# Optimization experiments

Measured on AMD Instinct MI355X. Metric: run time of the kernel, lower is better.

## Reference

```python
import jax, jax.numpy as jnp
import numpy as np

B, NX, NH, NY, K = 4096, 512, 512, 256, 8


def setup_inputs() -> dict:
    key = jax.random.key(0)
    k0, k1, k2, k3, k4, k5 = jax.random.split(key, 6)
    s = 1.0 / np.sqrt(NH)  # torch RNNCell init scale
    x = jax.random.normal(k0, (B, NX), jnp.float32)
    h = jax.random.normal(k1, (B, NH), jnp.float32)
    pi = jax.random.uniform(k2, (B, K), jnp.float32)
    pi = pi / pi.sum(axis=1, keepdims=True)  # __init_belief normalizes to sum 1
    W_ih = jax.random.uniform(k3, (K, NH, NX), jnp.float32, minval=-s, maxval=s)
    W_hh = jax.random.uniform(k4, (K, NH, NH), jnp.float32, minval=-s, maxval=s)
    W_out = jax.random.uniform(k5, (NY, NH), jnp.float32, minval=-s, maxval=s)
    return {"x": x, "h": h, "pi": pi, "W_ih": W_ih, "W_hh": W_hh, "W_out": W_out}


def reference(x, h, pi, W_ih, W_hh, W_out):
    # Per-state RNN cells (bias=False): h_k[:, :, k] = tanh(x @ W_ih[k].T + h @ W_hh[k].T)
    h_k = jnp.tanh(
        jnp.einsum('bx,knx->bnk', x, W_ih)
        + jnp.einsum('bh,knh->bnk', h, W_hh)
    )  # (B, NH, K)
    # out_k = out_layer applied per state: (B, NY, K)
    out_k = jnp.einsum('bnk,yn->byk', h_k, W_out)
    # belief-weighted soft combination of hidden states: states[b] = h_k[b] @ pi[b]
    h_mix = jnp.einsum('bnk,bk->bn', h_k, pi)  # (B, NH)
    out = h_mix @ W_out.T  # (B, NY)
    return (out, h_mix, out_k, h_k)
```

## Files before the change

### kernel.cpp

```cpp
#include <hip/hip_runtime.h>
#include <hip/hip_bf16.h>
#include <stdint.h>

typedef unsigned short u16;
typedef __attribute__((ext_vector_type(8))) short short8;
typedef __attribute__((ext_vector_type(4))) float f32x4;

#define BATCH 4096
#define OFF_OUT  0
#define OFF_HMIX (BATCH * 256)
#define OFF_OK   (OFF_HMIX + BATCH * 512)
#define OFF_HK   (OFF_OK + BATCH * 256 * 8)

#define WS_XB   0
#define WS_HB   (2097152)
#define WS_WIH  (4194304)
#define WS_WHH  (6291456)
#define WS_WOUT (8388608)
#define WS_T    (8519680)
#define WS_OB   (25296896)

__device__ __forceinline__ float b2f(u16 v) {
  union { uint32_t u; float f; } c; c.u = ((uint32_t)v) << 16; return c.f;
}
__device__ __forceinline__ u16 f2b(float f) {
  union { float f; uint32_t u; } c; c.f = f;
  uint32_t u = c.u;
  return (u16)((u + 0x7fffu + ((u >> 16) & 1u)) >> 16);
}

__device__ __forceinline__ void gload16(const u16* g, u16* l) {
  __builtin_amdgcn_global_load_lds(
      (const __attribute__((address_space(1))) void*)g,
      (__attribute__((address_space(3))) void*)l, 16, 0, 0);
}

__global__ __launch_bounds__(256) void k0_cvt(
    const float* __restrict__ x, const float* __restrict__ h,
    const float* __restrict__ Wih, const float* __restrict__ Whh,
    const float* __restrict__ Wout, u16* __restrict__ ws) {
  const int i = blockIdx.x * 256 + threadIdx.x;
  const float* src; int j; size_t dst;
  if      (i <  524288) { src = x;    j = i;           dst = WS_XB;   }
  else if (i < 1048576) { src = h;    j = i -  524288; dst = WS_HB;   }
  else if (i < 1572864) { src = Wih;  j = i - 1048576; dst = WS_WIH;  }
  else if (i < 2097152) { src = Whh;  j = i - 1572864; dst = WS_WHH;  }
  else                  { src = Wout; j = i - 2097152; dst = WS_WOUT; }
  const float4 v = ((const float4*)src)[j];
  ushort4 o;
  o.x = f2b(v.x); o.y = f2b(v.y); o.z = f2b(v.z); o.w = f2b(v.w);
  ((ushort4*)(ws + dst))[j] = o;
}

__global__ __launch_bounds__(256) void k1_gemm_tanh(
    const u16* __restrict__ xb, const u16* __restrict__ hb,
    const u16* __restrict__ Wih, const u16* __restrict__ Whh,
    u16* __restrict__ Tb) {
  __shared__ u16 S[128 * 136];
  u16* As = S;
  u16* Bs = S + 128 * 64;
  const int tid  = threadIdx.x;
  const int lane = tid & 63;
  const int w    = tid >> 6;
  const int wm   = w >> 1, wn = w & 1;
  const int row0 = blockIdx.x * 128;
  const int col0 = blockIdx.y * 128;
  const int kk   = col0 >> 9;
  const int nh0  = col0 & 511;
  const int sr   = tid >> 3;
  const int sc   = ((tid & 7) ^ ((tid >> 3) & 7)) * 8;
  const int ldsw = (w * 8) * 64;

  const u16* WihK = Wih + (size_t)kk * 512 * 512;
  const u16* WhhK = Whh + (size_t)kk * 512 * 512;

  f32x4 acc[4][4] = {};

  for (int kt = 0; kt < 16; ++kt) {
    const int kb = kt * 64;
    const u16* Asrc; const u16* Bsrc; int ko;
    if (kb < 512) { Asrc = xb; Bsrc = WihK; ko = kb; }
    else          { Asrc = hb; Bsrc = WhhK; ko = kb - 512; }
#pragma unroll
    for (int ro = 0; ro < 4; ++ro) {
      gload16(Asrc + (size_t)(row0 + ro * 32 + sr) * 512 + ko + sc, &As[ro * 32 * 64 + ldsw]);
      gload16(Bsrc + (size_t)(nh0  + ro * 32 + sr) * 512 + ko + sc, &Bs[ro * 32 * 64 + ldsw]);
    }
    __syncthreads();
    const int l7 = lane & 7, quad = lane >> 4, rl = lane & 15;
#pragma unroll
    for (int ks = 0; ks < 2; ++ks) {
      short8 af[4], bf[4];
      const int cs = ((ks * 4 + quad) ^ l7) * 8;
#pragma unroll
      for (int i = 0; i < 4; ++i)
        af[i] = *(const short8*)&As[(wm * 64 + i * 16 + rl) * 64 + cs];
#pragma unroll
      for (int j = 0; j < 4; ++j)
        bf[j] = *(const short8*)&Bs[(wn * 64 + j * 16 + rl) * 64 + cs];
#pragma unroll
      for (int i = 0; i < 4; ++i)
#pragma unroll
        for (int j = 0; j < 4; ++j)
          acc[i][j] = __builtin_amdgcn_mfma_f32_16x16x32_bf16(af[i], bf[j], acc[i][j], 0, 0, 0);
    }
    __syncthreads();
  }

  const int quad = lane >> 4, cl = lane & 15;
#pragma unroll
  for (int i = 0; i < 4; ++i)
#pragma unroll
    for (int j = 0; j < 4; ++j)
#pragma unroll
      for (int r = 0; r < 4; ++r) {
        const int row = wm * 64 + i * 16 + quad * 4 + r;
        const int col = wn * 64 + j * 16 + cl;
        const float v = acc[i][j][r];
        const float e = __expf(2.0f * v);
        S[row * 136 + col] = f2b(1.0f - 2.0f / (e + 1.0f));
      }
  __syncthreads();
#pragma unroll
  for (int it = 0; it < 8; ++it) {
    const int idx = it * 256 + tid;
    const int c = idx & 15;
    const int r = idx >> 4;
    *(short8*)&Tb[(size_t)(row0 + r) * 4096 + col0 + c * 8] =
        *(const short8*)&S[r * 136 + c * 8];
  }
}

__global__ __launch_bounds__(256) void k2_gemm_out(
    const u16* __restrict__ Tb, const u16* __restrict__ Wout,
    u16* __restrict__ Ob) {
  __shared__ u16 S[128 * 136];
  u16* As = S;
  u16* Bs = S + 128 * 64;
  const int tid  = threadIdx.x;
  const int lane = tid & 63;
  const int w    = tid >> 6;
  const int wm   = w >> 1, wn = w & 1;
  const int row0 = blockIdx.x * 128;
  const int y0   = blockIdx.y * 128;
  const int kk   = blockIdx.z;
  const int sr   = tid >> 3;
  const int sc   = ((tid & 7) ^ ((tid >> 3) & 7)) * 8;
  const int ldsw = (w * 8) * 64;

  f32x4 acc[4][4] = {};

  for (int kt = 0; kt < 8; ++kt) {
    const int kb = kt * 64;
#pragma unroll
    for (int ro = 0; ro < 4; ++ro) {
      gload16(Tb + (size_t)(row0 + ro * 32 + sr) * 4096 + kk * 512 + kb + sc,
              &As[ro * 32 * 64 + ldsw]);
      gload16(Wout + (size_t)(y0 + ro * 32 + sr) * 512 + kb + sc,
              &Bs[ro * 32 * 64 + ldsw]);
    }
    __syncthreads();
    const int l7 = lane & 7, quad = lane >> 4, rl = lane & 15;
#pragma unroll
    for (int ks = 0; ks < 2; ++ks) {
      short8 af[4], bf[4];
      const int cs = ((ks * 4 + quad) ^ l7) * 8;
#pragma unroll
      for (int i = 0; i < 4; ++i)
        af[i] = *(const short8*)&As[(wm * 64 + i * 16 + rl) * 64 + cs];
#pragma unroll
      for (int j = 0; j < 4; ++j)
        bf[j] = *(const short8*)&Bs[(wn * 64 + j * 16 + rl) * 64 + cs];
#pragma unroll
      for (int i = 0; i < 4; ++i)
#pragma unroll
        for (int j = 0; j < 4; ++j)
          acc[i][j] = __builtin_amdgcn_mfma_f32_16x16x32_bf16(af[i], bf[j], acc[i][j], 0, 0, 0);
    }
    __syncthreads();
  }

  const int quad = lane >> 4, cl = lane & 15;
#pragma unroll
  for (int i = 0; i < 4; ++i)
#pragma unroll
    for (int j = 0; j < 4; ++j)
#pragma unroll
      for (int r = 0; r < 4; ++r) {
        const int row = wm * 64 + i * 16 + quad * 4 + r;
        const int col = wn * 64 + j * 16 + cl;
        S[row * 136 + col] = f2b(acc[i][j][r]);
      }
  __syncthreads();
#pragma unroll
  for (int it = 0; it < 8; ++it) {
    const int idx = it * 256 + tid;
    const int c = idx & 15;
    const int r = idx >> 4;
    *(short8*)&Ob[(size_t)(row0 + r) * 2048 + kk * 256 + y0 + c * 8] =
        *(const short8*)&S[r * 136 + c * 8];
  }
}

__global__ __launch_bounds__(512) void k3_epi(const float* __restrict__ pi,
                                              const u16* __restrict__ Tb,
                                              const u16* __restrict__ Ob,
                                              float* __restrict__ dout) {
  const int b   = blockIdx.x;
  const int tid = threadIdx.x;

  float pif[8];
#pragma unroll
  for (int k = 0; k < 8; ++k) pif[k] = pi[b * 8 + k];

  float tv[8]; float hm = 0.0f;
#pragma unroll
  for (int k = 0; k < 8; ++k) {
    const float v = b2f(Tb[(size_t)b * 4096 + k * 512 + tid]);
    tv[k] = v; hm += pif[k] * v;
  }
  float4* tw = (float4*)&dout[OFF_HK + (size_t)b * 4096 + tid * 8];
  tw[0] = make_float4(tv[0], tv[1], tv[2], tv[3]);
  tw[1] = make_float4(tv[4], tv[5], tv[6], tv[7]);
  dout[OFF_HMIX + (size_t)b * 512 + tid] = hm;

  if (tid < 256) {
    float ov[8]; float om = 0.0f;
#pragma unroll
    for (int k = 0; k < 8; ++k) {
      const float v = b2f(Ob[(size_t)b * 2048 + k * 256 + tid]);
      ov[k] = v; om += pif[k] * v;
    }
    float4* ow = (float4*)&dout[OFF_OK + (size_t)b * 2048 + tid * 8];
    ow[0] = make_float4(ov[0], ov[1], ov[2], ov[3]);
    ow[1] = make_float4(ov[4], ov[5], ov[6], ov[7]);
    dout[OFF_OUT + (size_t)b * 256 + tid] = om;
  }
}

extern "C" void kernel_launch(void* const* d_in, const int* in_sizes, int n_in,
                              void* d_out, int out_size, void* d_ws, size_t ws_size,
                              hipStream_t stream) {
  const float* x    = (const float*)d_in[0];
  const float* h    = (const float*)d_in[1];
  const float* pi   = (const float*)d_in[2];
  const float* Wih  = (const float*)d_in[3];
  const float* Whh  = (const float*)d_in[4];
  const float* Wout = (const float*)d_in[5];
  float* out = (float*)d_out;
  u16* ws  = (u16*)d_ws;

  k0_cvt<<<dim3(8320), 256, 0, stream>>>(x, h, Wih, Whh, Wout, ws);
  k1_gemm_tanh<<<dim3(32, 32), 256, 0, stream>>>(
      ws + WS_XB, ws + WS_HB, ws + WS_WIH, ws + WS_WHH, ws + WS_T);
  k2_gemm_out<<<dim3(32, 2, 8), 256, 0, stream>>>(ws + WS_T, ws + WS_WOUT, ws + WS_OB);
  k3_epi<<<dim3(BATCH), 512, 0, stream>>>(pi, ws + WS_T, ws + WS_OB, out);
}
```

Measured before the change: 220.5 us.

## Rewrite gate GEMM with 256x256 tiles, double-buffered LDS and interleaved MFMA phases

The first GEMM kernel moves from 128x128 tiles with 4 waves to 256x256 tiles with 8 waves per block. It double-buffers the K tiles in 128KB of LDS and splits each K step into four phases that interleave staging loads, LDS reads and MFMA bursts, with raised wave priority during the MFMAs. A block-id swizzle remaps the 256 blocks for L2 locality, and the tanh epilogue is written out in two halves through LDS. The goal is to hide global-load latency and raise data reuse per loaded byte, at the cost of fewer blocks (256 on a large GPU), more registers and LDS, and the risk of barrier or waitcnt bugs.

```diff
diff --git a/kernel.cpp b/kernel.cpp
--- a/kernel.cpp
+++ b/kernel.cpp
@@ -52,82 +52,159 @@
   ((ushort4*)(ws + dst))[j] = o;
 }
 
-__global__ __launch_bounds__(256) void k1_gemm_tanh(
+__global__ __launch_bounds__(512, 2) void k1_gemm_tanh(
     const u16* __restrict__ xb, const u16* __restrict__ hb,
     const u16* __restrict__ Wih, const u16* __restrict__ Whh,
     u16* __restrict__ Tb) {
-  __shared__ u16 S[128 * 136];
-  u16* As = S;
-  u16* Bs = S + 128 * 64;
+  __shared__ u16 S[65536];
   const int tid  = threadIdx.x;
   const int lane = tid & 63;
   const int w    = tid >> 6;
-  const int wm   = w >> 1, wn = w & 1;
-  const int row0 = blockIdx.x * 128;
-  const int col0 = blockIdx.y * 128;
+  const int wm   = w >> 2;
+  const int wn   = w & 3;
+  const int quad = lane >> 4, rl = lane & 15, l7 = lane & 7;
+  const int sr   = tid >> 3;
+  const int sc   = ((tid & 7) ^ (sr & 7)) * 8;
+
+  const int wg  = blockIdx.x;
+  const int lin = ((wg & 7) << 5) | (wg >> 3);
+  const int bx  = lin & 15;
+  const int by  = lin >> 4;
+  const int row0 = bx * 256;
+  const int col0 = by * 256;
   const int kk   = col0 >> 9;
   const int nh0  = col0 & 511;
-  const int sr   = tid >> 3;
-  const int sc   = ((tid & 7) ^ ((tid >> 3) & 7)) * 8;
-  const int ldsw = (w * 8) * 64;
-
-  const u16* WihK = Wih + (size_t)kk * 512 * 512;
-  const u16* WhhK = Whh + (size_t)kk * 512 * 512;
-
-  f32x4 acc[4][4] = {};
-
-  for (int kt = 0; kt < 16; ++kt) {
-    const int kb = kt * 64;
-    const u16* Asrc; const u16* Bsrc; int ko;
-    if (kb < 512) { Asrc = xb; Bsrc = WihK; ko = kb; }
-    else          { Asrc = hb; Bsrc = WhhK; ko = kb - 512; }
-#pragma unroll
-    for (int ro = 0; ro < 4; ++ro) {
-      gload16(Asrc + (size_t)(row0 + ro * 32 + sr) * 512 + ko + sc, &As[ro * 32 * 64 + ldsw]);
-      gload16(Bsrc + (size_t)(nh0  + ro * 32 + sr) * 512 + ko + sc, &Bs[ro * 32 * 64 + ldsw]);
-    }
-    __syncthreads();
-    const int l7 = lane & 7, quad = lane >> 4, rl = lane & 15;
-#pragma unroll
-    for (int ks = 0; ks < 2; ++ks) {
-      short8 af[4], bf[4];
-      const int cs = ((ks * 4 + quad) ^ l7) * 8;
-#pragma unroll
-      for (int i = 0; i < 4; ++i)
-        af[i] = *(const short8*)&As[(wm * 64 + i * 16 + rl) * 64 + cs];
-#pragma unroll
-      for (int j = 0; j < 4; ++j)
-        bf[j] = *(const short8*)&Bs[(wn * 64 + j * 16 + rl) * 64 + cs];
-#pragma unroll
-      for (int i = 0; i < 4; ++i)
-#pragma unroll
-        for (int j = 0; j < 4; ++j)
-          acc[i][j] = __builtin_amdgcn_mfma_f32_16x16x32_bf16(af[i], bf[j], acc[i][j], 0, 0, 0);
-    }
-    __syncthreads();
-  }
-
-  const int quad = lane >> 4, cl = lane & 15;
-#pragma unroll
-  for (int i = 0; i < 4; ++i)
-#pragma unroll
-    for (int j = 0; j < 4; ++j)
-#pragma unroll
-      for (int r = 0; r < 4; ++r) {
-        const int row = wm * 64 + i * 16 + quad * 4 + r;
-        const int col = wn * 64 + j * 16 + cl;
-        const float v = acc[i][j][r];
-        const float e = __expf(2.0f * v);
-        S[row * 136 + col] = f2b(1.0f - 2.0f / (e + 1.0f));
-      }
-  __syncthreads();
-#pragma unroll
-  for (int it = 0; it < 8; ++it) {
-    const int idx = it * 256 + tid;
-    const int c = idx & 15;
-    const int r = idx >> 4;
-    *(short8*)&Tb[(size_t)(row0 + r) * 4096 + col0 + c * 8] =
-        *(const short8*)&S[r * 136 + c * 8];
+
+  const u16* const As2[2] = { xb, hb };
+  const u16* const Bs2[2] = { Wih + (size_t)kk * 262144, Whh + (size_t)kk * 262144 };
+
+  auto stage = [&](int tile, int region) {
+    if (tile >= 16) return;
+    const int g    = tile >> 3;
+    const int ko   = (tile & 7) * 64;
+    const int isB  = region >> 1;
+    const int half = region & 1;
+    const u16* src = isB ? Bs2[g] : As2[g];
+    const int r0   = (isB ? nh0 : row0) + half * 128;
+    u16* dst = S + (tile & 1) * 32768 + isB * 16384 + half * 8192;
+    const u16* s0 = src + (size_t)(r0 + sr) * 512 + ko + sc;
+    gload16(s0,            dst + tid * 8);
+    gload16(s0 + 64 * 512, dst + 4096 + tid * 8);
+  };
+
+  auto ldA = [&](int buf, int mi, int ks) -> short8 {
+    return *(const short8*)&S[buf * 32768 +
+                              (wm * 128 + mi * 16 + rl) * 64 +
+                              ((ks * 4 + quad) ^ l7) * 8];
+  };
+  auto ldB = [&](int buf, int j, int ks) -> short8 {
+    return *(const short8*)&S[buf * 32768 + 16384 +
+                              (wn * 64 + j * 16 + rl) * 64 +
+                              ((ks * 4 + quad) ^ l7) * 8];
+  };
+
+  f32x4 acc[8][4] = {};
+  short8 af[4][2], bf[4][2];
+
+  stage(0, 0); stage(0, 1); stage(0, 2); stage(0, 3); stage(1, 0);
+  asm volatile("s_waitcnt vmcnt(2)" ::: "memory");
+  __builtin_amdgcn_s_barrier();
+
+#pragma unroll 1
+  for (int t = 0; t < 16; ++t) {
+    const int buf = t & 1;
+
+#pragma unroll
+    for (int m = 0; m < 4; ++m) { af[m][0] = ldA(buf, m, 0); af[m][1] = ldA(buf, m, 1); }
+#pragma unroll
+    for (int j = 0; j < 2; ++j) { bf[j][0] = ldB(buf, j, 0); bf[j][1] = ldB(buf, j, 1); }
+    stage(t + 1, 1);
+    __builtin_amdgcn_s_barrier();
+    asm volatile("s_waitcnt lgkmcnt(0)" ::: "memory");
+    __builtin_amdgcn_s_setprio(1);
+#pragma unroll
+    for (int m = 0; m < 4; ++m)
+#pragma unroll
+      for (int n = 0; n < 2; ++n)
+#pragma unroll
+        for (int ks = 0; ks < 2; ++ks)
+          acc[m][n] = __builtin_amdgcn_mfma_f32_16x16x32_bf16(af[m][ks], bf[n][ks], acc[m][n], 0, 0, 0);
+    __builtin_amdgcn_s_setprio(0);
+    __builtin_amdgcn_s_barrier();
+
+#pragma unroll
+    for (int j = 2; j < 4; ++j) { bf[j][0] = ldB(buf, j, 0); bf[j][1] = ldB(buf, j, 1); }
+    stage(t + 1, 2);
+    __builtin_amdgcn_s_barrier();
+    asm volatile("s_waitcnt lgkmcnt(0)" ::: "memory");
+    __builtin_amdgcn_s_setprio(1);
+#pragma unroll
+    for (int m = 0; m < 4; ++m)
+#pragma unroll
+      for (int n = 2; n < 4; ++n)
+#pragma unroll
+        for (int ks = 0; ks < 2; ++ks)
+          acc[m][n] = __builtin_amdgcn_mfma_f32_16x16x32_bf16(af[m][ks], bf[n][ks], acc[m][n], 0, 0, 0);
+    __builtin_amdgcn_s_setprio(0);
+    __builtin_amdgcn_s_barrier();
+
+#pragma unroll
+    for (int m = 0; m < 4; ++m) { af[m][0] = ldA(buf, 4 + m, 0); af[m][1] = ldA(buf, 4 + m, 1); }
+    stage(t + 1, 3);
+    __builtin_amdgcn_s_barrier();
+    asm volatile("s_waitcnt lgkmcnt(0)" ::: "memory");
+    __builtin_amdgcn_s_setprio(1);
+#pragma unroll
+    for (int m = 0; m < 4; ++m)
+#pragma unroll
+      for (int n = 2; n < 4; ++n)
+#pragma unroll
+        for (int ks = 0; ks < 2; ++ks)
+          acc[4 + m][n] = __builtin_amdgcn_mfma_f32_16x16x32_bf16(af[m][ks], bf[n][ks], acc[4 + m][n], 0, 0, 0);
+    __builtin_amdgcn_s_setprio(0);
+    __builtin_amdgcn_s_barrier();
+
+    stage(t + 2, 0);
+    __builtin_amdgcn_s_barrier();
+    __builtin_amdgcn_s_setprio(1);
+#pragma unroll
+    for (int m = 0; m < 4; ++m)
+#pragma unroll
+      for (int n = 0; n < 2; ++n)
+#pragma unroll
+        for (int ks = 0; ks < 2; ++ks)
+          acc[4 + m][n] = __builtin_amdgcn_mfma_f32_16x16x32_bf16(af[m][ks], bf[n][ks], acc[4 + m][n], 0, 0, 0);
+    __builtin_amdgcn_s_setprio(0);
+    if (t < 14) asm volatile("s_waitcnt vmcnt(2)" ::: "memory");
+    else        asm volatile("s_waitcnt vmcnt(0)" ::: "memory");
+    __builtin_amdgcn_s_barrier();
+  }
+
+#pragma unroll 1
+  for (int hp = 0; hp < 2; ++hp) {
+    if (wm == hp) {
+#pragma unroll
+      for (int m = 0; m < 8; ++m)
+#pragma unroll
+        for (int n = 0; n < 4; ++n)
+#pragma unroll
+          for (int r = 0; r < 4; ++r) {
+            const int lr = m * 16 + quad * 4 + r;
+            const float v = acc[m][n][r];
+            const float e = __expf(2.0f * v);
+            S[lr * 264 + wn * 64 + n * 16 + rl] = f2b(1.0f - 2.0f / (e + 1.0f));
+          }
+    }
+    asm volatile("s_waitcnt lgkmcnt(0)" ::: "memory");
+    __builtin_amdgcn_s_barrier();
+#pragma unroll
+    for (int p = 0; p < 8; ++p) {
+      const int idx = p * 512 + tid;
+      const int c = idx & 31, rr = idx >> 5;
+      *(short8*)&Tb[(size_t)(row0 + hp * 128 + rr) * 4096 + col0 + c * 8] =
+          *(const short8*)&S[rr * 264 + c * 8];
+    }
+    __builtin_amdgcn_s_barrier();
   }
 }
 
@@ -251,7 +328,7 @@
   u16* ws  = (u16*)d_ws;
 
   k0_cvt<<<dim3(8320), 256, 0, stream>>>(x, h, Wih, Whh, Wout, ws);
-  k1_gemm_tanh<<<dim3(32, 32), 256, 0, stream>>>(
+  k1_gemm_tanh<<<dim3(256), 512, 0, stream>>>(
       ws + WS_XB, ws + WS_HB, ws + WS_WIH, ws + WS_WHH, ws + WS_T);
   k2_gemm_out<<<dim3(32, 2, 8), 256, 0, stream>>>(ws + WS_T, ws + WS_WOUT, ws + WS_OB);
   k3_epi<<<dim3(BATCH), 512, 0, stream>>>(pi, ws + WS_T, ws + WS_OB, out);
```

Result: faster. 215.4 us (-2.3%).
